# Kernel optimization log

Measured on AMD Instinct MI355X. Metric: run time of the kernel, lower is better.

Reference implementation:

```python
import jax, jax.numpy as jnp
import numpy as np

B, N, E = 64, 256, 512   # batch, leaves (power of 2), embed_size
D, U = 512, 512          # tree_size, units (controller size == units)


def setup_inputs() -> dict:
    key = jax.random.key(0)
    ks = jax.random.split(key, 11)
    sc = lambda k, shape: jax.random.normal(k, shape, dtype=jnp.float32) * 0.05
    return {
        "inputs": jax.random.normal(ks[0], (B, N, E), dtype=jnp.float32),
        "h0": sc(ks[1], (B, U)),
        "c0": sc(ks[2], (B, U)),
        "W_t": sc(ks[3], (E, D)),          # Transformer
        "W_j": sc(ks[4], (2 * D, D)),      # Join
        "W_s": sc(ks[5], (D + U, 1)),      # Search
        "W_h": sc(ks[6], (D + U, D)),      # Write candidate
        "W_T": sc(ks[7], (D + U, 1)),      # Write gate
        "kernel": sc(ks[8], (E, 4 * U)),   # LSTM input kernel (i,f,c,o)
        "rec_kernel": sc(ks[9], (U, 4 * U)),
        "bias": jnp.zeros((4 * U,), jnp.float32),
    }


def reference(inputs, h0, c0, W_t, W_j, W_s, W_h, W_T, kernel, rec_kernel, bias):
    b, n, e = inputs.shape
    control = h0  # control = previous LSTM hidden state

    # --- leaf embed: Transformer, batched over all leaves ---
    leaf_h = jax.nn.relu(jnp.einsum('bne,ed->bnd', inputs, W_t))  # [B,N,D]

    # --- refresh: bottom-up join, batched per tree level ---
    levels = [leaf_h]
    h = leaf_h
    while h.shape[1] > 1:
        pair = jnp.concatenate([h[:, 0::2], h[:, 1::2]], axis=-1)  # [B,m/2,2D]
        h = jax.nn.relu(jnp.einsum('bmk,kd->bmd', pair, W_j))
        levels.append(h)

    # --- retrieve: top-down search producing leaf attentions ---
    # Searches all use refresh-time h (parent search happens before any
    # update in its subtree), so a level-batched top-down pass is exact.
    attn = jnp.ones((b, 1, 1), inputs.dtype)
    for lvl in range(len(levels) - 1, 0, -1):
        node_h = levels[lvl]                     # [B,m,D]
        m = node_h.shape[1]
        ctrl = jnp.broadcast_to(control[:, None, :], (b, m, control.shape[-1]))
        mr = jax.nn.sigmoid(jnp.einsum('bmk,ko->bmo',
                                       jnp.concatenate([node_h, ctrl], -1), W_s))  # [B,m,1]
        # children interleave: left gets attn*(1-mr), right gets attn*mr
        attn = jnp.concatenate([attn * (1.0 - mr), attn * mr], axis=-1).reshape(b, 2 * m, 1)

    tree_out = jnp.sum(attn * inputs, axis=1)  # [B,E] soft-retrieved leaf value

    # --- write update of leaf memories, batched over all leaves ---
    ctrl = jnp.broadcast_to(control[:, None, :], (b, n, control.shape[-1]))
    data = jnp.concatenate([leaf_h, ctrl], -1)                     # [B,N,D+U]
    cand = jax.nn.sigmoid(jnp.einsum('bnk,kd->bnd', data, W_h))
    upd = jax.nn.sigmoid(jnp.einsum('bnk,ko->bno', data, W_T))
    written = upd * cand + (1.0 - upd) * leaf_h
    leaf_h_new = attn * written + (1.0 - attn) * leaf_h            # [B,N,D]

    # --- LSTM cell update (keras LSTMCell gate order i,f,c,o) ---
    z = tree_out @ kernel + h0 @ rec_kernel + bias
    zi, zf, zg, zo = jnp.split(z, 4, axis=-1)
    c_new = jax.nn.sigmoid(zf) * c0 + jax.nn.sigmoid(zi) * jnp.tanh(zg)
    h_new = jax.nn.sigmoid(zo) * jnp.tanh(c_new)
    return h_new, c_new, leaf_h_new
```

## Files before the change

### kernel.cpp

```cpp
#include <hip/hip_runtime.h>
#include <hip/hip_bf16.h>
#include <cstdint>
#include <cstddef>


__device__ __forceinline__ float sigmoidf_(float x) { return 1.0f / (1.0f + __expf(-x)); }

typedef __attribute__((ext_vector_type(8))) short bf16x8;
typedef __attribute__((ext_vector_type(4))) float f32x4;

__device__ __forceinline__ void load_lds16(const void* g, void* l) {
  __builtin_amdgcn_global_load_lds((const __attribute__((address_space(1))) void*)g,
                                   (__attribute__((address_space(3))) void*)l, 16, 0, 0);
}

__global__ __launch_bounds__(256)
void cvt_bf16(const float* __restrict__ x, __hip_bfloat16* __restrict__ y, int n) {
  int i = (blockIdx.x * 256 + threadIdx.x) * 4;
  if (i < n) {
    float4 v = *(const float4*)(x + i);
    y[i]     = __float2bfloat16(v.x);
    y[i + 1] = __float2bfloat16(v.y);
    y[i + 2] = __float2bfloat16(v.z);
    y[i + 3] = __float2bfloat16(v.w);
  }
}

__global__ __launch_bounds__(256)
void tconv_all(const float* __restrict__ W_t, const float* __restrict__ W_j,
               const float* __restrict__ W_h,
               __hip_bfloat16* __restrict__ Wt_t, __hip_bfloat16* __restrict__ Wt_j,
               __hip_bfloat16* __restrict__ Wt_h) {
  const int z = blockIdx.z;
  if (z != 1 && blockIdx.x >= 16) return;
  const int K = (z == 1) ? 1024 : 512;
  const float* W = (z == 0) ? W_t : ((z == 1) ? W_j : W_h);
  __hip_bfloat16* Wt = (z == 0) ? Wt_t : ((z == 1) ? Wt_j : Wt_h);
  __shared__ float sh[32][33];
  const int tx = threadIdx.x & 31, ty = threadIdx.x >> 5;
  const int k0 = blockIdx.x * 32, n0 = blockIdx.y * 32;
#pragma unroll
  for (int i = 0; i < 4; ++i)
    sh[ty + i * 8][tx] = W[(size_t)(k0 + ty + i * 8) * 512 + n0 + tx];
  __syncthreads();
#pragma unroll
  for (int i = 0; i < 4; ++i)
    Wt[(size_t)(n0 + ty + i * 8) * K + k0 + tx] = __float2bfloat16(sh[tx][ty + i * 8]);
}

template<int MODE>
__global__ __launch_bounds__(256)
void mfma_gemm(const __hip_bfloat16* __restrict__ A, const __hip_bfloat16* __restrict__ Bt,
               int M, int K,
               __hip_bfloat16* __restrict__ Cb, float* __restrict__ Cf,
               const float* __restrict__ ctrl_h, const float* __restrict__ attn,
               const float* __restrict__ upd, const __hip_bfloat16* __restrict__ leaf) {
  __shared__ __align__(16) __hip_bfloat16 Asm[128 * 32];
  __shared__ __align__(16) __hip_bfloat16 Bsm[128 * 32];
  const int tid = threadIdx.x;
  const int wave = tid >> 6, lane = tid & 63;
  const int bm = blockIdx.y * 128, bn = blockIdx.x * 128;
  const int wm = (wave >> 1) * 64, wn = (wave & 1) * 64;
  const int q = lane >> 4, lr = lane & 15;

  f32x4 acc[4][4] = {};

  const int c0 = wave * 128 + lane, c1 = c0 + 64;
  const size_t ga0 = (size_t)(bm + (c0 >> 2)) * K + (c0 & 3) * 8;
  const size_t ga1 = (size_t)(bm + (c1 >> 2)) * K + (c1 & 3) * 8;
  const size_t gb0 = (size_t)(bn + (c0 >> 2)) * K + (c0 & 3) * 8;
  const size_t gb1 = (size_t)(bn + (c1 >> 2)) * K + (c1 & 3) * 8;
  __hip_bfloat16* la0 = Asm + wave * 1024;
  __hip_bfloat16* la1 = Asm + wave * 1024 + 512;
  __hip_bfloat16* lb0 = Bsm + wave * 1024;
  __hip_bfloat16* lb1 = Bsm + wave * 1024 + 512;

  for (int k0v = 0; k0v < K; k0v += 32) {
    load_lds16(A + ga0 + k0v, la0);
    load_lds16(A + ga1 + k0v, la1);
    load_lds16(Bt + gb0 + k0v, lb0);
    load_lds16(Bt + gb1 + k0v, lb1);
    __syncthreads();
    bf16x8 af[4], bfr[4];
#pragma unroll
    for (int mt = 0; mt < 4; ++mt)
      af[mt] = *(const bf16x8*)(Asm + (wm + mt * 16 + lr) * 32 + q * 8);
#pragma unroll
    for (int nt = 0; nt < 4; ++nt)
      bfr[nt] = *(const bf16x8*)(Bsm + (wn + nt * 16 + lr) * 32 + q * 8);
#pragma unroll
    for (int mt = 0; mt < 4; ++mt)
#pragma unroll
      for (int nt = 0; nt < 4; ++nt)
        acc[mt][nt] = __builtin_amdgcn_mfma_f32_16x16x32_bf16(af[mt], bfr[nt], acc[mt][nt], 0, 0, 0);
    __syncthreads();
  }

  if (MODE == 0) {
#pragma unroll
    for (int mt = 0; mt < 4; ++mt) {
      const int rbase = bm + wm + mt * 16 + q * 4;
#pragma unroll
      for (int nt = 0; nt < 4; ++nt) {
        const int col = bn + wn + nt * 16 + lr;
#pragma unroll
        for (int r = 0; r < 4; ++r) {
          const int row = rbase + r;
          if (row < M)
            Cb[(size_t)row * 512 + col] = __float2bfloat16(fmaxf(acc[mt][nt][r], 0.f));
        }
      }
    }
  } else {
#pragma unroll
    for (int mt = 0; mt < 4; ++mt) {
      const int rbase = bm + wm + mt * 16 + q * 4;
#pragma unroll
      for (int r = 0; r < 4; ++r) {
        const int row = rbase + r;
        const float a = attn[row];
        const float u = upd[row];
        const int bidx = row >> 8;
#pragma unroll
        for (int nt = 0; nt < 4; ++nt) {
          const int col = bn + wn + nt * 16 + lr;
          const float cand = sigmoidf_(acc[mt][nt][r] + ctrl_h[(size_t)bidx * 512 + col]);
          const float lf = __bfloat162float(leaf[(size_t)row * 512 + col]);
          const float w = u * cand + (1.f - u) * lf;
          Cf[(size_t)row * 512 + col] = a * w + (1.f - a) * lf;
        }
      }
    }
  }
}

__global__ __launch_bounds__(256)
void join_level(const __hip_bfloat16* __restrict__ in, __hip_bfloat16* __restrict__ outp,
                const __hip_bfloat16* __restrict__ Wt_j, int m_out) {
  const int wave = threadIdx.x >> 6, lane = threadIdx.x & 63;
  const int q = lane >> 4, lr = lane & 15;
  const int ntile = blockIdx.x * 4 + wave;
  const int b = blockIdx.y;
  const int arow = (lr < m_out) ? lr : (m_out - 1);
  const __hip_bfloat16* ap = in + ((size_t)b * (2 * m_out) + 2 * arow) * 512 + q * 8;
  const __hip_bfloat16* bp = Wt_j + (size_t)(ntile * 16 + lr) * 1024 + q * 8;
  f32x4 acc = {0.f, 0.f, 0.f, 0.f};
#pragma unroll 8
  for (int k0 = 0; k0 < 1024; k0 += 32) {
    bf16x8 a  = *(const bf16x8*)(ap + k0);
    bf16x8 bb = *(const bf16x8*)(bp + k0);
    acc = __builtin_amdgcn_mfma_f32_16x16x32_bf16(a, bb, acc, 0, 0, 0);
  }
  const int col = ntile * 16 + lr;
#pragma unroll
  for (int r = 0; r < 4; ++r) {
    const int row = q * 4 + r;
    if (row < m_out)
      outp[((size_t)b * m_out + row) * 512 + col] = __float2bfloat16(fmaxf(acc[r], 0.f));
  }
}

__global__ __launch_bounds__(256)
void gemv512(const __hip_bfloat16* __restrict__ X, const float* __restrict__ w,
             const float* __restrict__ addv, float* __restrict__ y,
             int apply_sig) {
  const int wave = threadIdx.x >> 6, lane = threadIdx.x & 63;
  const int row = blockIdx.x * 4 + wave;
  union { bf16x8 v; __hip_bfloat16 e[8]; } u;
  u.v = *(const bf16x8*)(X + (size_t)row * 512 + lane * 8);
  const float* wp = w + lane * 8;
  float p = 0.f;
#pragma unroll
  for (int j = 0; j < 8; ++j) p += __bfloat162float(u.e[j]) * wp[j];
#pragma unroll
  for (int off = 32; off > 0; off >>= 1) p += __shfl_down(p, off);
  if (lane == 0)
    y[row] = apply_sig ? sigmoidf_(p + addv[row >> 8]) : p;
}

__global__ __launch_bounds__(256)
void prep_ctrl(const float* __restrict__ h0, const float* __restrict__ W_T,
               float* __restrict__ ctrlT) {
  const int b = blockIdx.x, tid = threadIdx.x;
  __shared__ float part[256];
  float p = 0.f;
  for (int i = tid; i < 512; i += 256) p += h0[b * 512 + i] * W_T[512 + i];
  part[tid] = p; __syncthreads();
  for (int s = 128; s > 0; s >>= 1) { if (tid < s) part[tid] += part[tid + s]; __syncthreads(); }
  if (tid == 0) ctrlT[b] = part[0];
}

__global__ __launch_bounds__(256)
void propagate(const float* __restrict__ sc, const float* __restrict__ h0,
               const float* __restrict__ W_s, float* __restrict__ attn_out) {
  const int b = blockIdx.x, tid = threadIdx.x;
  __shared__ float part[256], attn_sh[256], newattn[256];
  __shared__ float scs;
  float p = 0.f;
  for (int i = tid; i < 512; i += 256) p += h0[b * 512 + i] * W_s[512 + i];
  part[tid] = p; __syncthreads();
  for (int s = 128; s > 0; s >>= 1) { if (tid < s) part[tid] += part[tid + s]; __syncthreads(); }
  if (tid == 0) { scs = part[0]; attn_sh[0] = 1.f; }
  __syncthreads();
  const int row_off[9] = {0, 0, 8192, 12288, 14336, 15360, 15872, 16128, 16256};
#pragma unroll
  for (int l = 8; l >= 1; --l) {
    const int m = 256 >> l;
    if (tid < m) {
      const float mr = sigmoidf_(sc[row_off[l] + b * m + tid] + scs);
      const float a = attn_sh[tid];
      newattn[2 * tid]     = a * (1.f - mr);
      newattn[2 * tid + 1] = a * mr;
    }
    __syncthreads();
    if (tid < 2 * m) attn_sh[tid] = newattn[tid];
    __syncthreads();
  }
  attn_out[b * 256 + tid] = attn_sh[tid];
}

__global__ __launch_bounds__(256)
void tree_part(const float* __restrict__ inputs, const float* __restrict__ attn,
               float* __restrict__ tp) {
  const int s = blockIdx.x, b = blockIdx.y;
  const int tid = threadIdx.x;
  __shared__ float a_sh[64];
  if (tid < 64) a_sh[tid] = attn[b * 256 + s * 64 + tid];
  __syncthreads();
  float acc0 = 0.f, acc1 = 0.f;
  const float* base = inputs + ((size_t)b * 256 + s * 64) * 512;
  for (int nn = 0; nn < 64; ++nn) {
    const float a = a_sh[nn];
    const float* row = base + (size_t)nn * 512;
    acc0 += a * row[tid];
    acc1 += a * row[tid + 256];
  }
  tp[((size_t)s * 64 + b) * 512 + tid]       = acc0;
  tp[((size_t)s * 64 + b) * 512 + tid + 256] = acc1;
}

__global__ __launch_bounds__(256)
void tree_reduce(const float* __restrict__ tp, float* __restrict__ tre) {
  const int i = blockIdx.x * 256 + threadIdx.x;
  tre[i] = tp[i] + tp[32768 + i] + tp[65536 + i] + tp[98304 + i];
}

__global__ __launch_bounds__(256)
void ctrl_gemm(const float* __restrict__ h0, const float* __restrict__ W_h,
               float* __restrict__ chp) {
  const int col = blockIdx.x * 256 + threadIdx.x;
  const int b   = blockIdx.y;
  const int z   = blockIdx.z;
  __shared__ float hsh[128];
  if (threadIdx.x < 128) hsh[threadIdx.x] = h0[b * 512 + z * 128 + threadIdx.x];
  __syncthreads();
  const float* Wp = W_h + (size_t)(512 + z * 128) * 512 + col;
  float s = 0.f;
#pragma unroll 8
  for (int k = 0; k < 128; ++k) s += hsh[k] * Wp[(size_t)k * 512];
  chp[((size_t)z * 64 + b) * 512 + col] = s;
}

__global__ __launch_bounds__(256)
void ctrl_reduce(const float* __restrict__ chp, float* __restrict__ ch) {
  const int i = blockIdx.x * 256 + threadIdx.x;
  ch[i] = chp[i] + chp[32768 + i] + chp[65536 + i] + chp[98304 + i];
}

__global__ __launch_bounds__(256)
void lstm_gemm_splitk(const float* __restrict__ tre, const float* __restrict__ h0,
                      const float* __restrict__ kern, const float* __restrict__ rec,
                      float* __restrict__ Zp) {
  const int tid = threadIdx.x;
  const int col = blockIdx.x * 256 + tid;
  const int b0 = blockIdx.y * 4;
  const int z = blockIdx.z;
  const float* X = (z < 4) ? tre : h0;
  const float* W = (z < 4) ? (kern + (size_t)z * 128 * 2048)
                           : (rec + (size_t)(z - 4) * 128 * 2048);
  const int koff = (z & 3) * 128;
  __shared__ float xs[4][128];
  for (int i = tid; i < 512; i += 256) {
    int bb = i >> 7, k = i & 127;
    xs[bb][k] = X[(b0 + bb) * 512 + koff + k];
  }
  __syncthreads();
  float a0 = 0.f, a1 = 0.f, a2 = 0.f, a3 = 0.f;
#pragma unroll 8
  for (int k = 0; k < 128; ++k) {
    const float w = W[(size_t)k * 2048 + col];
    a0 += xs[0][k] * w;
    a1 += xs[1][k] * w;
    a2 += xs[2][k] * w;
    a3 += xs[3][k] * w;
  }
  Zp[((size_t)z * 64 + b0 + 0) * 2048 + col] = a0;
  Zp[((size_t)z * 64 + b0 + 1) * 2048 + col] = a1;
  Zp[((size_t)z * 64 + b0 + 2) * 2048 + col] = a2;
  Zp[((size_t)z * 64 + b0 + 3) * 2048 + col] = a3;
}

__global__ __launch_bounds__(256)
void lstm_combine(const float* __restrict__ Zp, const float* __restrict__ bias,
                  const float* __restrict__ c0,
                  float* __restrict__ out_h, float* __restrict__ out_c) {
  const int i = blockIdx.x * 256 + threadIdx.x;
  const int b = i >> 9, u = i & 511;
  float zi = bias[u], zf = bias[512 + u], zg = bias[1024 + u], zo = bias[1536 + u];
#pragma unroll
  for (int z = 0; z < 8; ++z) {
    const size_t base = ((size_t)z * 64 + b) * 2048;
    zi += Zp[base + u];
    zf += Zp[base + 512 + u];
    zg += Zp[base + 1024 + u];
    zo += Zp[base + 1536 + u];
  }
  const float c = sigmoidf_(zf) * c0[i] + sigmoidf_(zi) * tanhf(zg);
  out_h[i] = sigmoidf_(zo) * tanhf(c);
  out_c[i] = c;
}

extern "C" void kernel_launch(void* const* d_in, const int* in_sizes, int n_in,
                              void* d_out, int out_size, void* d_ws, size_t ws_size,
                              hipStream_t stream) {
  const float* inputs = (const float*)d_in[0];
  const float* h0     = (const float*)d_in[1];
  const float* c0     = (const float*)d_in[2];
  const float* W_t    = (const float*)d_in[3];
  const float* W_j    = (const float*)d_in[4];
  const float* W_s    = (const float*)d_in[5];
  const float* W_h    = (const float*)d_in[6];
  const float* W_T    = (const float*)d_in[7];
  const float* kern   = (const float*)d_in[8];
  const float* rec    = (const float*)d_in[9];
  const float* bias   = (const float*)d_in[10];
  float* out = (float*)d_out;

  char* p = (char*)d_ws;
  __hip_bfloat16* in_bf     = (__hip_bfloat16*)p; p += 16777216;
  __hip_bfloat16* leaf_bf   = (__hip_bfloat16*)p; p += 16777216;
  __hip_bfloat16* levels_bf = (__hip_bfloat16*)p; p += 16842752;
  __hip_bfloat16* Wt_t      = (__hip_bfloat16*)p; p += 524288;
  __hip_bfloat16* Wt_j      = (__hip_bfloat16*)p; p += 1048576;
  __hip_bfloat16* Wt_h      = (__hip_bfloat16*)p; p += 524288;
  float* attn  = (float*)p; p += 65536;
  float* upd   = (float*)p; p += 65536;
  float* tre   = (float*)p; p += 131072;
  float* chp   = (float*)p; p += 524288;
  float* ch    = (float*)p; p += 131072;
  float* Zp    = (float*)p; p += 4194304;
  float* sc    = (float*)p; p += 65536;
  float* ctrlT = (float*)p; p += 4096;
  float* tp    = (float*)p; p += 524288;

  cvt_bf16<<<8192, 256, 0, stream>>>(inputs, in_bf, 8388608);
  tconv_all<<<dim3(32, 16, 3), 256, 0, stream>>>(W_t, W_j, W_h, Wt_t, Wt_j, Wt_h);
  ctrl_gemm<<<dim3(2, 64, 4), 256, 0, stream>>>(h0, W_h, chp);
  ctrl_reduce<<<128, 256, 0, stream>>>(chp, ch);
  prep_ctrl<<<64, 256, 0, stream>>>(h0, W_T, ctrlT);

  mfma_gemm<0><<<dim3(4, 128), 256, 0, stream>>>(in_bf, Wt_t, 16384, 512,
                                                 leaf_bf, nullptr, nullptr, nullptr, nullptr, nullptr);
  gemv512<<<4096, 256, 0, stream>>>(leaf_bf, W_T, ctrlT, upd, 1);

  const int lvl_off_h[9] = {0, 0, 4194304, 6291456, 7340032,
                            7864320, 8126464, 8257536, 8323072};
  const __hip_bfloat16* Aptr = leaf_bf;
  for (int l = 1; l <= 3; ++l) {
    const int M = 64 * (256 >> l);
    __hip_bfloat16* Cl = levels_bf + lvl_off_h[l];
    mfma_gemm<0><<<dim3(4, M / 128), 256, 0, stream>>>(Aptr, Wt_j, M, 1024,
                                                       Cl, nullptr, nullptr, nullptr, nullptr, nullptr);
    Aptr = Cl;
  }
  for (int l = 4; l <= 8; ++l) {
    join_level<<<dim3(8, 64), 256, 0, stream>>>(levels_bf + lvl_off_h[l - 1],
                                                levels_bf + lvl_off_h[l], Wt_j, 256 >> l);
  }

  gemv512<<<4080, 256, 0, stream>>>(levels_bf, W_s, nullptr, sc, 0);
  propagate<<<64, 256, 0, stream>>>(sc, h0, W_s, attn);

  tree_part<<<dim3(4, 64), 256, 0, stream>>>(inputs, attn, tp);
  tree_reduce<<<128, 256, 0, stream>>>(tp, tre);

  mfma_gemm<1><<<dim3(4, 128), 256, 0, stream>>>(leaf_bf, Wt_h, 16384, 512,
                                                 nullptr, out + 65536, ch, attn, upd, leaf_bf);
  lstm_gemm_splitk<<<dim3(8, 16, 8), 256, 0, stream>>>(tre, h0, kern, rec, Zp);
  lstm_combine<<<128, 256, 0, stream>>>(Zp, bias, c0, out, out + 32768);
}
```

Baseline: 345.1 us.

## Fuse fp32-to-bf16 conversion into leaf GEMM, repack join levels, merge gemvs

Removes the separate cvt_bf16 pass by having the leaf-embed GEMM read fp32 inputs directly, convert them in registers and store them to LDS. This avoids writing and re-reading a 16 MB bf16 copy, at the cost of synchronous loads in place of async global_load_lds for the A operand. The small join levels are retiled so each wave handles a dense 16-row tile of contiguous paired rows instead of one padded batch per block, which removes wasted rows. The two gemv launches (update gate and search scores) are merged into a single launch.

Result: faster. 332.5 us (-3.6%).

```diff
diff --git a/kernel.cpp b/kernel.cpp
--- a/kernel.cpp
+++ b/kernel.cpp
@@ -12,18 +12,6 @@
 __device__ __forceinline__ void load_lds16(const void* g, void* l) {
   __builtin_amdgcn_global_load_lds((const __attribute__((address_space(1))) void*)g,
                                    (__attribute__((address_space(3))) void*)l, 16, 0, 0);
-}
-
-__global__ __launch_bounds__(256)
-void cvt_bf16(const float* __restrict__ x, __hip_bfloat16* __restrict__ y, int n) {
-  int i = (blockIdx.x * 256 + threadIdx.x) * 4;
-  if (i < n) {
-    float4 v = *(const float4*)(x + i);
-    y[i]     = __float2bfloat16(v.x);
-    y[i + 1] = __float2bfloat16(v.y);
-    y[i + 2] = __float2bfloat16(v.z);
-    y[i + 3] = __float2bfloat16(v.w);
-  }
 }
 
 __global__ __launch_bounds__(256)
@@ -48,10 +36,10 @@
     Wt[(size_t)(n0 + ty + i * 8) * K + k0 + tx] = __float2bfloat16(sh[tx][ty + i * 8]);
 }
 
-template<int MODE>
-__global__ __launch_bounds__(256)
-void mfma_gemm(const __hip_bfloat16* __restrict__ A, const __hip_bfloat16* __restrict__ Bt,
-               int M, int K,
+template<int MODE, bool AFP32>
+__global__ __launch_bounds__(256)
+void mfma_gemm(const __hip_bfloat16* __restrict__ A, const float* __restrict__ Af,
+               const __hip_bfloat16* __restrict__ Bt, int M, int K,
                __hip_bfloat16* __restrict__ Cb, float* __restrict__ Cf,
                const float* __restrict__ ctrl_h, const float* __restrict__ attn,
                const float* __restrict__ upd, const __hip_bfloat16* __restrict__ leaf) {
@@ -76,8 +64,20 @@
   __hip_bfloat16* lb1 = Bsm + wave * 1024 + 512;
 
   for (int k0v = 0; k0v < K; k0v += 32) {
-    load_lds16(A + ga0 + k0v, la0);
-    load_lds16(A + ga1 + k0v, la1);
+    if (AFP32) {
+#pragma unroll
+      for (int it = 0; it < 4; ++it) {
+        const int c = it * 256 + tid;
+        const int row = c >> 3, kc = c & 7;
+        float4 v = *(const float4*)(Af + (size_t)(bm + row) * K + k0v + kc * 4);
+        __hip_bfloat16 h[4] = {__float2bfloat16(v.x), __float2bfloat16(v.y),
+                               __float2bfloat16(v.z), __float2bfloat16(v.w)};
+        *(ushort4*)(Asm + row * 32 + kc * 4) = *(ushort4*)h;
+      }
+    } else {
+      load_lds16(A + ga0 + k0v, la0);
+      load_lds16(A + ga1 + k0v, la1);
+    }
     load_lds16(Bt + gb0 + k0v, lb0);
     load_lds16(Bt + gb1 + k0v, lb1);
     __syncthreads();
@@ -136,13 +136,12 @@
 
 __global__ __launch_bounds__(256)
 void join_level(const __hip_bfloat16* __restrict__ in, __hip_bfloat16* __restrict__ outp,
-                const __hip_bfloat16* __restrict__ Wt_j, int m_out) {
+                const __hip_bfloat16* __restrict__ Wt_j) {
   const int wave = threadIdx.x >> 6, lane = threadIdx.x & 63;
   const int q = lane >> 4, lr = lane & 15;
-  const int ntile = blockIdx.x * 4 + wave;
-  const int b = blockIdx.y;
-  const int arow = (lr < m_out) ? lr : (m_out - 1);
-  const __hip_bfloat16* ap = in + ((size_t)b * (2 * m_out) + 2 * arow) * 512 + q * 8;
+  const int tile = blockIdx.x * 4 + wave;
+  const int mtile = tile >> 5, ntile = tile & 31;
+  const __hip_bfloat16* ap = in + (size_t)(mtile * 16 + lr) * 1024 + q * 8;
   const __hip_bfloat16* bp = Wt_j + (size_t)(ntile * 16 + lr) * 1024 + q * 8;
   f32x4 acc = {0.f, 0.f, 0.f, 0.f};
 #pragma unroll 8
@@ -152,20 +151,24 @@
     acc = __builtin_amdgcn_mfma_f32_16x16x32_bf16(a, bb, acc, 0, 0, 0);
   }
   const int col = ntile * 16 + lr;
-#pragma unroll
-  for (int r = 0; r < 4; ++r) {
-    const int row = q * 4 + r;
-    if (row < m_out)
-      outp[((size_t)b * m_out + row) * 512 + col] = __float2bfloat16(fmaxf(acc[r], 0.f));
-  }
-}
-
-__global__ __launch_bounds__(256)
-void gemv512(const __hip_bfloat16* __restrict__ X, const float* __restrict__ w,
-             const float* __restrict__ addv, float* __restrict__ y,
-             int apply_sig) {
+  const int orow = mtile * 16 + q * 4;
+#pragma unroll
+  for (int r = 0; r < 4; ++r)
+    outp[(size_t)(orow + r) * 512 + col] = __float2bfloat16(fmaxf(acc[r], 0.f));
+}
+
+__global__ __launch_bounds__(256)
+void gemv_dual(const __hip_bfloat16* __restrict__ leaf,
+               const __hip_bfloat16* __restrict__ levels,
+               const float* __restrict__ W_T, const float* __restrict__ W_s,
+               const float* __restrict__ ctrlT,
+               float* __restrict__ upd, float* __restrict__ sc) {
   const int wave = threadIdx.x >> 6, lane = threadIdx.x & 63;
-  const int row = blockIdx.x * 4 + wave;
+  const int bid = blockIdx.x;
+  const bool is_upd = bid < 4096;
+  const int row = (is_upd ? bid : (bid - 4096)) * 4 + wave;
+  const __hip_bfloat16* X = is_upd ? leaf : levels;
+  const float* w = is_upd ? W_T : W_s;
   union { bf16x8 v; __hip_bfloat16 e[8]; } u;
   u.v = *(const bf16x8*)(X + (size_t)row * 512 + lane * 8);
   const float* wp = w + lane * 8;
@@ -174,8 +177,10 @@
   for (int j = 0; j < 8; ++j) p += __bfloat162float(u.e[j]) * wp[j];
 #pragma unroll
   for (int off = 32; off > 0; off >>= 1) p += __shfl_down(p, off);
-  if (lane == 0)
-    y[row] = apply_sig ? sigmoidf_(p + addv[row >> 8]) : p;
+  if (lane == 0) {
+    if (is_upd) upd[row] = sigmoidf_(p + ctrlT[row >> 8]);
+    else        sc[row] = p;
+  }
 }
 
 __global__ __launch_bounds__(256)
@@ -337,7 +342,6 @@
   float* out = (float*)d_out;
 
   char* p = (char*)d_ws;
-  __hip_bfloat16* in_bf     = (__hip_bfloat16*)p; p += 16777216;
   __hip_bfloat16* leaf_bf   = (__hip_bfloat16*)p; p += 16777216;
   __hip_bfloat16* levels_bf = (__hip_bfloat16*)p; p += 16842752;
   __hip_bfloat16* Wt_t      = (__hip_bfloat16*)p; p += 524288;
@@ -353,15 +357,14 @@
   float* ctrlT = (float*)p; p += 4096;
   float* tp    = (float*)p; p += 524288;
 
-  cvt_bf16<<<8192, 256, 0, stream>>>(inputs, in_bf, 8388608);
   tconv_all<<<dim3(32, 16, 3), 256, 0, stream>>>(W_t, W_j, W_h, Wt_t, Wt_j, Wt_h);
   ctrl_gemm<<<dim3(2, 64, 4), 256, 0, stream>>>(h0, W_h, chp);
   ctrl_reduce<<<128, 256, 0, stream>>>(chp, ch);
   prep_ctrl<<<64, 256, 0, stream>>>(h0, W_T, ctrlT);
 
-  mfma_gemm<0><<<dim3(4, 128), 256, 0, stream>>>(in_bf, Wt_t, 16384, 512,
-                                                 leaf_bf, nullptr, nullptr, nullptr, nullptr, nullptr);
-  gemv512<<<4096, 256, 0, stream>>>(leaf_bf, W_T, ctrlT, upd, 1);
+  mfma_gemm<0, true><<<dim3(4, 128), 256, 0, stream>>>(
+      nullptr, inputs, Wt_t, 16384, 512,
+      leaf_bf, nullptr, nullptr, nullptr, nullptr, nullptr);
 
   const int lvl_off_h[9] = {0, 0, 4194304, 6291456, 7340032,
                             7864320, 8126464, 8257536, 8323072};
@@ -369,23 +372,26 @@
   for (int l = 1; l <= 3; ++l) {
     const int M = 64 * (256 >> l);
     __hip_bfloat16* Cl = levels_bf + lvl_off_h[l];
-    mfma_gemm<0><<<dim3(4, M / 128), 256, 0, stream>>>(Aptr, Wt_j, M, 1024,
-                                                       Cl, nullptr, nullptr, nullptr, nullptr, nullptr);
+    mfma_gemm<0, false><<<dim3(4, M / 128), 256, 0, stream>>>(
+        Aptr, nullptr, Wt_j, M, 1024,
+        Cl, nullptr, nullptr, nullptr, nullptr, nullptr);
     Aptr = Cl;
   }
   for (int l = 4; l <= 8; ++l) {
-    join_level<<<dim3(8, 64), 256, 0, stream>>>(levels_bf + lvl_off_h[l - 1],
-                                                levels_bf + lvl_off_h[l], Wt_j, 256 >> l);
-  }
-
-  gemv512<<<4080, 256, 0, stream>>>(levels_bf, W_s, nullptr, sc, 0);
+    const int m_out = 256 >> l;
+    join_level<<<32 * m_out, 256, 0, stream>>>(levels_bf + lvl_off_h[l - 1],
+                                               levels_bf + lvl_off_h[l], Wt_j);
+  }
+
+  gemv_dual<<<8176, 256, 0, stream>>>(leaf_bf, levels_bf, W_T, W_s, ctrlT, upd, sc);
   propagate<<<64, 256, 0, stream>>>(sc, h0, W_s, attn);
 
   tree_part<<<dim3(4, 64), 256, 0, stream>>>(inputs, attn, tp);
   tree_reduce<<<128, 256, 0, stream>>>(tp, tre);
 
-  mfma_gemm<1><<<dim3(4, 128), 256, 0, stream>>>(leaf_bf, Wt_h, 16384, 512,
-                                                 nullptr, out + 65536, ch, attn, upd, leaf_bf);
+  mfma_gemm<1, false><<<dim3(4, 128), 256, 0, stream>>>(
+      leaf_bf, nullptr, Wt_h, 16384, 512,
+      nullptr, out + 65536, ch, attn, upd, leaf_bf);
   lstm_gemm_splitk<<<dim3(8, 16, 8), 256, 0, stream>>>(tre, h0, kern, rec, Zp);
   lstm_combine<<<128, 256, 0, stream>>>(Zp, bias, c0, out, out + 32768);
 }
```
